# Performance work log

Hardware: AMD Instinct MI355X
Metric: run time of the kernel (lower is better)

Reference implementation:

```python
import jax, jax.numpy as jnp
import numpy as np

EMBED_DIM = 1024
NUM_HEADS = 16
HEAD_DIM = EMBED_DIM // NUM_HEADS
LN_EPS = 1e-5


def setup_inputs() -> dict:
    key = jax.random.key(0)
    ks = jax.random.split(key, 6)
    b, s, d = 2, 2048, EMBED_DIM
    scale = 1.0 / np.sqrt(d)
    x = jax.random.normal(ks[0], (b, s, d), dtype=jnp.float32)
    w_qkv = jax.random.normal(ks[1], (d, 3 * d), dtype=jnp.float32) * scale
    b_qkv = jax.random.normal(ks[2], (3 * d,), dtype=jnp.float32) * 0.02
    w_out = jax.random.normal(ks[3], (d, d), dtype=jnp.float32) * scale
    b_out = jax.random.normal(ks[4], (d,), dtype=jnp.float32) * 0.02
    gamma = jnp.ones((d,), dtype=jnp.float32)
    ln_beta = jnp.zeros((d,), dtype=jnp.float32)
    beta = jax.random.normal(ks[5], (), dtype=jnp.float32) * 0.1
    return {"x": x, "w_qkv": w_qkv, "b_qkv": b_qkv, "w_out": w_out,
            "b_out": b_out, "gamma": gamma, "ln_beta": ln_beta, "beta": beta}


def _layernorm(x, gamma, ln_beta):
    mu = jnp.mean(x, axis=-1, keepdims=True)
    var = jnp.mean(jnp.square(x - mu), axis=-1, keepdims=True)
    return (x - mu) * jax.lax.rsqrt(var + LN_EPS) * gamma + ln_beta


def reference(x, w_qkv, b_qkv, w_out, b_out, gamma, ln_beta, beta):
    b, s, d = x.shape
    h, hd = NUM_HEADS, HEAD_DIM
    residual = x
    xn = _layernorm(x, gamma, ln_beta)
    qkv = xn @ w_qkv + b_qkv                       # [b, s, 3d]
    qkv = qkv.reshape(b, s, 3, h, hd)
    q = jnp.transpose(qkv[:, :, 0], (0, 2, 1, 3))  # [b, h, s, hd]
    k = jnp.transpose(qkv[:, :, 1], (0, 2, 1, 3))
    v = jnp.transpose(qkv[:, :, 2], (0, 2, 1, 3))
    attn = jnp.einsum('bhqd,bhkd->bhqk', q, k) / np.sqrt(hd)
    idx = jnp.arange(s)
    dist = jnp.abs(idx[None, :] - idx[:, None]).astype(attn.dtype)  # [s, s]
    attn = attn + beta * jnp.log1p(dist)[None, None, :, :]
    probs = jax.nn.softmax(attn, axis=-1)
    ctx = jnp.einsum('bhqk,bhkd->bhqd', probs, v)  # [b, h, s, hd]
    ctx = jnp.transpose(ctx, (0, 2, 1, 3)).reshape(b, s, d)
    return residual + ctx @ w_out + b_out
```

## Files before the change

### kernel.cpp

```cpp
#include <hip/hip_runtime.h>

#define SEQ 2048
#define DIM 1024
#define NHEAD 16
#define HDIM 64
#define NTOK 4096
#define N3D 3072

typedef __attribute__((ext_vector_type(8))) short bf16x8;
typedef __attribute__((ext_vector_type(4))) float floatx4;
typedef __attribute__((ext_vector_type(4))) unsigned short ushortx4;

__device__ __forceinline__ unsigned short f2bf(float f) {
    unsigned int u = __builtin_bit_cast(unsigned int, f);
    u += 0x7FFFu + ((u >> 16) & 1u);
    return (unsigned short)(u >> 16);
}

__device__ __forceinline__ void async_copy16(const void* g, const void* l) {
    __builtin_amdgcn_global_load_lds(
        (const __attribute__((address_space(1))) unsigned int*)(unsigned long long)g,
        (__attribute__((address_space(3))) unsigned int*)(unsigned int)(unsigned long long)l,
        16, 0, 0);
}

#define MFMA_BF16(a, b, c) __builtin_amdgcn_mfma_f32_16x16x32_bf16((a), (b), (c), 0, 0, 0)

__global__ __launch_bounds__(256)
void prep_kernel(const float* __restrict__ w_qkv, unsigned short* __restrict__ wqkvT,
                 const float* __restrict__ w_out, unsigned short* __restrict__ woutT,
                 const float* __restrict__ x, const float* __restrict__ gamma,
                 const float* __restrict__ lnb, unsigned short* __restrict__ xn,
                 const float* __restrict__ betap, float* __restrict__ logt_g) {
    const int bid = blockIdx.x;
    const int tid = threadIdx.x;
    if (bid >= 8192) {
        const float betaV = betap[0];
        const float L2E = 1.44269504f;
        int i = (bid - 8192) * 256 + tid;
        logt_g[i] = betaV * log1pf((float)i) * L2E - 20.0f;
        logt_g[i + 1024] = betaV * log1pf((float)(i + 1024)) * L2E - 20.0f;
        return;
    }
    if (bid < 4096) {
        __shared__ float tile[32][33];
        const float* src; unsigned short* dst; int cols, bx, by;
        if (bid < 3072) { src = w_qkv; dst = wqkvT; cols = N3D; bx = bid % 96; by = bid / 96; }
        else { int t = bid - 3072; src = w_out; dst = woutT; cols = DIM; bx = t & 31; by = t >> 5; }
        const int c0 = bx * 32, r0 = by * 32;
        const int tx = tid & 31, ty = tid >> 5;
        for (int i = 0; i < 4; ++i) {
            int r = ty + i * 8;
            tile[r][tx] = src[(size_t)(r0 + r) * cols + c0 + tx];
        }
        __syncthreads();
        for (int i = 0; i < 4; ++i) {
            int rr = ty + i * 8;
            dst[(size_t)(c0 + rr) * DIM + r0 + tx] = f2bf(tile[tx][rr]);
        }
    } else {
        const int row = bid - 4096;
        const float* xr = x + (size_t)row * DIM;
        float4 v = ((const float4*)xr)[tid];
        float s = v.x + v.y + v.z + v.w;
        float s2 = v.x * v.x + v.y * v.y + v.z * v.z + v.w * v.w;
        for (int off = 1; off < 64; off <<= 1) {
            s += __shfl_xor(s, off, 64);
            s2 += __shfl_xor(s2, off, 64);
        }
        __shared__ float red[8];
        const int wave = tid >> 6, lane = tid & 63;
        if (lane == 0) { red[wave] = s; red[4 + wave] = s2; }
        __syncthreads();
        s = red[0] + red[1] + red[2] + red[3];
        s2 = red[4] + red[5] + red[6] + red[7];
        const float mu = s * (1.0f / DIM);
        const float var = s2 * (1.0f / DIM) - mu * mu;
        const float rstd = rsqrtf(var + 1e-5f);
        float4 g = ((const float4*)gamma)[tid];
        float4 bb = ((const float4*)lnb)[tid];
        unsigned short* o = xn + (size_t)row * DIM + tid * 4;
        o[0] = f2bf((v.x - mu) * rstd * g.x + bb.x);
        o[1] = f2bf((v.y - mu) * rstd * g.y + bb.y);
        o[2] = f2bf((v.z - mu) * rstd * g.z + bb.z);
        o[3] = f2bf((v.w - mu) * rstd * g.w + bb.w);
    }
}

__global__ __launch_bounds__(512)
void qkv_gemm(const unsigned short* __restrict__ A, const unsigned short* __restrict__ Bt,
              const float* __restrict__ bias, unsigned short* __restrict__ qo,
              unsigned short* __restrict__ ko, unsigned short* __restrict__ vTo) {
    __shared__ unsigned short Asm[2][256 * 64];
    __shared__ unsigned short Bsm[2][192 * 64];
    const int tid = threadIdx.x;
    const int wave = tid >> 6, lane = tid & 63;
    const int quad = lane >> 4, r16 = lane & 15;
    const int flat = blockIdx.x;
    const int xcd = flat & 7, c = flat >> 3;
    const int mt = (xcd >> 1) * 4 + (c >> 3);
    const int nt = (xcd & 1) * 8 + (c & 7);
    const int m0 = mt * 256, n0 = nt * 192;
    const int wm = (wave & 1) * 128, wn = (wave >> 1) * 48;
    floatx4 acc[8][3] = {};
    for (int p = 0; p < 4; ++p) {
        int s = tid + p * 512;
        async_copy16(A + (size_t)(m0 + (s >> 3)) * DIM + ((s & 7) << 3), &Asm[0][s * 8]);
    }
    for (int p = 0; p < 3; ++p) {
        int s = tid + p * 512;
        async_copy16(Bt + (size_t)(n0 + (s >> 3)) * DIM + ((s & 7) << 3), &Bsm[0][s * 8]);
    }
    __syncthreads();
    for (int it = 0; it < 16; ++it) {
        const int cur = it & 1;
        if (it + 1 < 16) {
            const int k1 = (it + 1) * 64;
            for (int p = 0; p < 4; ++p) {
                int s = tid + p * 512;
                async_copy16(A + (size_t)(m0 + (s >> 3)) * DIM + k1 + ((s & 7) << 3),
                             &Asm[cur ^ 1][s * 8]);
            }
            for (int p = 0; p < 3; ++p) {
                int s = tid + p * 512;
                async_copy16(Bt + (size_t)(n0 + (s >> 3)) * DIM + k1 + ((s & 7) << 3),
                             &Bsm[cur ^ 1][s * 8]);
            }
        }
        for (int h = 0; h < 2; ++h) {
            bf16x8 af[8], bfr[3];
            for (int i = 0; i < 8; ++i)
                af[i] = *(const bf16x8*)(&Asm[cur][(wm + i * 16 + r16) * 64 + h * 32 + quad * 8]);
            for (int j = 0; j < 3; ++j)
                bfr[j] = *(const bf16x8*)(&Bsm[cur][(wn + j * 16 + r16) * 64 + h * 32 + quad * 8]);
            for (int i = 0; i < 8; ++i)
                for (int j = 0; j < 3; ++j)
                    acc[i][j] = MFMA_BF16(af[i], bfr[j], acc[i][j]);
        }
        __syncthreads();
    }
    for (int j = 0; j < 3; ++j) {
        int n = n0 + wn + j * 16 + r16;
        float bn = bias[n];
        int part = n >> 10, nn = n & 1023;
        int head = nn >> 6, hdi = nn & 63;
        for (int i = 0; i < 8; ++i) {
            int mbase = m0 + wm + i * 16 + quad * 4;
            int bIdx = mbase >> 11, sIdx = mbase & 2047;
            if (part == 2) {
                ushortx4 pack;
                for (int e = 0; e < 4; ++e) pack[e] = f2bf(acc[i][j][e] + bn);
                *(ushortx4*)(vTo + ((size_t)(bIdx * NHEAD + head) * HDIM + hdi) * SEQ + sIdx) = pack;
            } else {
                unsigned short* dst = (part == 0) ? qo : ko;
                for (int e = 0; e < 4; ++e)
                    dst[((size_t)(bIdx * NHEAD + head) * SEQ + sIdx + e) * HDIM + hdi] =
                        f2bf(acc[i][j][e] + bn);
            }
        }
    }
}

__global__ __launch_bounds__(512)
void attn_kernel(const unsigned short* __restrict__ qg, const unsigned short* __restrict__ kg,
                 const unsigned short* __restrict__ vTg, const float* __restrict__ logt,
                 unsigned short* __restrict__ ctx) {
    __shared__ unsigned short QP[128][72];
    __shared__ unsigned short Kd[2][64 * 64];
    __shared__ unsigned short Vd[2][64 * 64];

    const int tid = threadIdx.x;
    const int wave = tid >> 6, lane = tid & 63;
    const int quad = lane >> 4, r16 = lane & 15;
    const int flat = blockIdx.y * 16 + blockIdx.x;
    const int swz = (flat & 7) * 64 + (flat >> 3);
    const int bh = swz >> 4, qt = swz & 15;
    const int qBase = qt * 128;
    const float L2E = 1.44269504f;
    const float c1 = 0.125f * L2E;

    const unsigned short* qptr = qg + ((size_t)bh * SEQ + qBase) * HDIM;
    for (int s = tid; s < 1024; s += 512) {
        int r = s >> 3, c8 = (s & 7) << 3;
        *(bf16x8*)(&QP[r][c8]) = *(const bf16x8*)(qptr + r * HDIM + c8);
    }

    const int sr = tid >> 3;
    const int scg = (tid & 7) ^ (sr & 7);
    const unsigned short* kbh = kg + (size_t)bh * SEQ * HDIM;
    const unsigned short* vbh = vTg + (size_t)bh * HDIM * SEQ;
    async_copy16(kbh + (size_t)sr * HDIM + scg * 8, &Kd[0][tid * 8]);
    async_copy16(vbh + (size_t)sr * SEQ + scg * 8, &Vd[0][tid * 8]);
    __syncthreads();

    bf16x8 qf0 = *(const bf16x8*)(&QP[wave * 16 + r16][quad * 8]);
    bf16x8 qf1 = *(const bf16x8*)(&QP[wave * 16 + r16][32 + quad * 8]);

    const bf16x8 onesv = {0x3F80, 0x3F80, 0x3F80, 0x3F80, 0x3F80, 0x3F80, 0x3F80, 0x3F80};

    floatx4 o[5] = {};
    const int qWaveBase = qBase + wave * 16;
    const int qrT = qWaveBase + r16;

    for (int kt0 = 0; kt0 < SEQ; kt0 += 64) {
        const int buf = (kt0 >> 6) & 1;
        if (kt0 + 64 < SEQ) {
            async_copy16(kbh + (size_t)(kt0 + 64 + sr) * HDIM + scg * 8, &Kd[buf ^ 1][tid * 8]);
            async_copy16(vbh + (size_t)sr * SEQ + kt0 + 64 + scg * 8, &Vd[buf ^ 1][tid * 8]);
        }

        floatx4 sc[4];
        __builtin_amdgcn_s_setprio(1);
        for (int ct = 0; ct < 4; ++ct) {
            int rK = ct * 16 + r16;
            const unsigned short* kb = &Kd[buf][rK * 64];
            bf16x8 kf0 = *(const bf16x8*)(kb + ((quad ^ (rK & 7)) << 3));
            bf16x8 kf1 = *(const bf16x8*)(kb + (((quad ^ 4) ^ (rK & 7)) << 3));
            floatx4 z = {0.f, 0.f, 0.f, 0.f};
            z = MFMA_BF16(kf0, qf0, z);
            z = MFMA_BF16(kf1, qf1, z);
            sc[ct] = z;
        }
        __builtin_amdgcn_s_setprio(0);
        for (int ct = 0; ct < 4; ++ct) {
            const int keyTile = kt0 + ct * 16;
            const int kbase = keyTile + quad * 4;
            if (qWaveBase >= keyTile + 16) {
                const float* lp = &logt[qrT - kbase - 3];
                for (int i = 0; i < 4; ++i)
                    sc[ct][i] = __builtin_amdgcn_exp2f(sc[ct][i] * c1 + lp[3 - i]);
            } else if (keyTile >= qWaveBase + 16) {
                const float* lp = &logt[kbase - qrT];
                for (int i = 0; i < 4; ++i)
                    sc[ct][i] = __builtin_amdgcn_exp2f(sc[ct][i] * c1 + lp[i]);
            } else {
                for (int i = 0; i < 4; ++i) {
                    int dist = qrT - (kbase + i);
                    dist = dist < 0 ? -dist : dist;
                    sc[ct][i] = __builtin_amdgcn_exp2f(sc[ct][i] * c1 + logt[dist]);
                }
            }
        }
        {
            unsigned short* prow = &QP[wave * 16 + r16][0];
            for (int ct = 0; ct < 4; ++ct) {
                unsigned int lo, hi;
                asm("v_cvt_pk_bf16_f32 %0, %1, %2" : "=v"(lo) : "v"(sc[ct][0]), "v"(sc[ct][1]));
                asm("v_cvt_pk_bf16_f32 %0, %1, %2" : "=v"(hi) : "v"(sc[ct][2]), "v"(sc[ct][3]));
                uint2 pk; pk.x = lo; pk.y = hi;
                *(uint2*)(prow + ct * 16 + quad * 4) = pk;
            }
        }
        bf16x8 pf0 = *(const bf16x8*)(&QP[wave * 16 + r16][quad * 8]);
        bf16x8 pf1 = *(const bf16x8*)(&QP[wave * 16 + r16][32 + quad * 8]);
        __builtin_amdgcn_s_setprio(1);
        for (int nt = 0; nt < 4; ++nt) {
            int rV = nt * 16 + r16;
            const unsigned short* vb = &Vd[buf][rV * 64];
            bf16x8 vf0 = *(const bf16x8*)(vb + ((quad ^ (rV & 7)) << 3));
            bf16x8 vf1 = *(const bf16x8*)(vb + (((quad ^ 4) ^ (rV & 7)) << 3));
            o[nt] = MFMA_BF16(pf0, vf0, o[nt]);
            o[nt] = MFMA_BF16(pf1, vf1, o[nt]);
        }
        o[4] = MFMA_BF16(pf0, onesv, o[4]);
        o[4] = MFMA_BF16(pf1, onesv, o[4]);
        __builtin_amdgcn_s_setprio(0);

        __syncthreads();
    }

    const int b_ = bh >> 4, h_ = bh & 15;
    for (int i = 0; i < 4; ++i) {
        float inv = 1.0f / o[4][i];
        int qi = qBase + wave * 16 + quad * 4 + i;
        for (int nt = 0; nt < 4; ++nt) {
            int d = nt * 16 + r16;
            ctx[((size_t)(b_ * SEQ + qi)) * DIM + h_ * HDIM + d] = f2bf(o[nt][i] * inv);
        }
    }
}

__global__ __launch_bounds__(256)
void out_gemm(const unsigned short* __restrict__ A, const unsigned short* __restrict__ Bt,
              const float* __restrict__ bias, const float* __restrict__ resid,
              float* __restrict__ out) {
    __shared__ unsigned short Asm[2][128 * 64];
    __shared__ unsigned short Bsm[2][64 * 64];
    const int tid = threadIdx.x;
    const int wave = tid >> 6, lane = tid & 63;
    const int quad = lane >> 4, r16 = lane & 15;
    const int flat = blockIdx.y * 16 + blockIdx.x;
    const int swz = (flat & 7) * 64 + (flat >> 3);
    const int m0 = (swz >> 4) * 128, n0 = (swz & 15) * 64;
    const int wm = (wave & 1) * 64, wn = (wave >> 1) * 32;
    floatx4 acc[4][2] = {};
    for (int p = 0; p < 4; ++p) {
        int s = tid + p * 256;
        async_copy16(A + (size_t)(m0 + (s >> 3)) * DIM + ((s & 7) << 3), &Asm[0][s * 8]);
    }
    for (int p = 0; p < 2; ++p) {
        int s = tid + p * 256;
        async_copy16(Bt + (size_t)(n0 + (s >> 3)) * DIM + ((s & 7) << 3), &Bsm[0][s * 8]);
    }
    __syncthreads();
    for (int it = 0; it < 16; ++it) {
        const int cur = it & 1;
        if (it + 1 < 16) {
            const int k1 = (it + 1) * 64;
            for (int p = 0; p < 4; ++p) {
                int s = tid + p * 256;
                async_copy16(A + (size_t)(m0 + (s >> 3)) * DIM + k1 + ((s & 7) << 3),
                             &Asm[cur ^ 1][s * 8]);
            }
            for (int p = 0; p < 2; ++p) {
                int s = tid + p * 256;
                async_copy16(Bt + (size_t)(n0 + (s >> 3)) * DIM + k1 + ((s & 7) << 3),
                             &Bsm[cur ^ 1][s * 8]);
            }
        }
        for (int h = 0; h < 2; ++h) {
            bf16x8 af[4], bfr[2];
            for (int i = 0; i < 4; ++i)
                af[i] = *(const bf16x8*)(&Asm[cur][(wm + i * 16 + r16) * 64 + h * 32 + quad * 8]);
            for (int j = 0; j < 2; ++j)
                bfr[j] = *(const bf16x8*)(&Bsm[cur][(wn + j * 16 + r16) * 64 + h * 32 + quad * 8]);
            for (int i = 0; i < 4; ++i)
                for (int j = 0; j < 2; ++j)
                    acc[i][j] = MFMA_BF16(af[i], bfr[j], acc[i][j]);
        }
        __syncthreads();
    }
    for (int i = 0; i < 4; ++i)
        for (int j = 0; j < 2; ++j)
            for (int e = 0; e < 4; ++e) {
                int m = m0 + wm + i * 16 + quad * 4 + e;
                int n = n0 + wn + j * 16 + r16;
                out[(size_t)m * DIM + n] = acc[i][j][e] + bias[n] + resid[(size_t)m * DIM + n];
            }
}

extern "C" void kernel_launch(void* const* d_in, const int* in_sizes, int n_in,
                              void* d_out, int out_size, void* d_ws, size_t ws_size,
                              hipStream_t stream) {
    const float* x     = (const float*)d_in[0];
    const float* w_qkv = (const float*)d_in[1];
    const float* b_qkv = (const float*)d_in[2];
    const float* w_out = (const float*)d_in[3];
    const float* b_out = (const float*)d_in[4];
    const float* gamma = (const float*)d_in[5];
    const float* ln_b  = (const float*)d_in[6];
    const float* beta  = (const float*)d_in[7];
    float* out = (float*)d_out;

    char* ws = (char*)d_ws;
    const size_t MB = 1u << 20;
    unsigned short* xn    = (unsigned short*)(ws);
    unsigned short* wqkvT = (unsigned short*)(ws + 8 * MB);
    unsigned short* woutT = (unsigned short*)(ws + 14 * MB);
    unsigned short* qb    = (unsigned short*)(ws + 16 * MB);
    unsigned short* kb    = (unsigned short*)(ws + 24 * MB);
    unsigned short* vTb   = (unsigned short*)(ws + 32 * MB);
    float* logt_g         = (float*)(ws + 40 * MB);
    unsigned short* ctx   = xn;

    prep_kernel<<<8196, 256, 0, stream>>>(w_qkv, wqkvT, w_out, woutT, x, gamma, ln_b, xn,
                                          beta, logt_g);
    qkv_gemm<<<256, 512, 0, stream>>>(xn, wqkvT, b_qkv, qb, kb, vTb);
    attn_kernel<<<dim3(SEQ / 128, 32), 512, 0, stream>>>(qb, kb, vTb, logt_g, ctx);
    out_gemm<<<dim3(16, 32), 256, 0, stream>>>(ctx, woutT, b_out, x, out);
}
```

Measured before the change: 203.0 us.

## Process 32 query rows per wave in attention to reuse K/V fragments

Doubles the query tile per block to 256 rows, so each wave computes two 16-row query groups against the same K/V tiles loaded from LDS. Q fragments are loaded straight from global memory into registers instead of being staged through shared memory. The grid is halved to 256 blocks. The aim is to cut LDS reads and global K/V traffic per unit of work. In exchange, register pressure is higher and there are fewer blocks to hide latency.

```diff
diff --git a/kernel.cpp b/kernel.cpp
--- a/kernel.cpp
+++ b/kernel.cpp
@@ -165,25 +165,26 @@
 void attn_kernel(const unsigned short* __restrict__ qg, const unsigned short* __restrict__ kg,
                  const unsigned short* __restrict__ vTg, const float* __restrict__ logt,
                  unsigned short* __restrict__ ctx) {
-    __shared__ unsigned short QP[128][72];
+    __shared__ unsigned short QP[256][72];
     __shared__ unsigned short Kd[2][64 * 64];
     __shared__ unsigned short Vd[2][64 * 64];
 
     const int tid = threadIdx.x;
     const int wave = tid >> 6, lane = tid & 63;
     const int quad = lane >> 4, r16 = lane & 15;
-    const int flat = blockIdx.y * 16 + blockIdx.x;
-    const int swz = (flat & 7) * 64 + (flat >> 3);
-    const int bh = swz >> 4, qt = swz & 15;
-    const int qBase = qt * 128;
+    const int flat = blockIdx.x;
+    const int swz = (flat & 7) * 32 + (flat >> 3);
+    const int bh = swz >> 3, qt = swz & 7;
+    const int qBase = qt * 256;
     const float L2E = 1.44269504f;
     const float c1 = 0.125f * L2E;
 
     const unsigned short* qptr = qg + ((size_t)bh * SEQ + qBase) * HDIM;
-    for (int s = tid; s < 1024; s += 512) {
-        int r = s >> 3, c8 = (s & 7) << 3;
-        *(bf16x8*)(&QP[r][c8]) = *(const bf16x8*)(qptr + r * HDIM + c8);
-    }
+    const int qr0 = wave * 32 + r16;
+    bf16x8 qf0a = *(const bf16x8*)(qptr + qr0 * HDIM + quad * 8);
+    bf16x8 qf1a = *(const bf16x8*)(qptr + qr0 * HDIM + 32 + quad * 8);
+    bf16x8 qf0b = *(const bf16x8*)(qptr + (qr0 + 16) * HDIM + quad * 8);
+    bf16x8 qf1b = *(const bf16x8*)(qptr + (qr0 + 16) * HDIM + 32 + quad * 8);
 
     const int sr = tid >> 3;
     const int scg = (tid & 7) ^ (sr & 7);
@@ -193,14 +194,15 @@
     async_copy16(vbh + (size_t)sr * SEQ + scg * 8, &Vd[0][tid * 8]);
     __syncthreads();
 
-    bf16x8 qf0 = *(const bf16x8*)(&QP[wave * 16 + r16][quad * 8]);
-    bf16x8 qf1 = *(const bf16x8*)(&QP[wave * 16 + r16][32 + quad * 8]);
-
     const bf16x8 onesv = {0x3F80, 0x3F80, 0x3F80, 0x3F80, 0x3F80, 0x3F80, 0x3F80, 0x3F80};
 
-    floatx4 o[5] = {};
-    const int qWaveBase = qBase + wave * 16;
-    const int qrT = qWaveBase + r16;
+    floatx4 oa[5] = {}, ob[5] = {};
+    const int qWB0 = qBase + wave * 32;
+    const int qWB1 = qWB0 + 16;
+    const int qrTa = qWB0 + r16;
+    const int qrTb = qWB1 + r16;
+    unsigned short* prowA = &QP[wave * 32 + r16][0];
+    unsigned short* prowB = &QP[wave * 32 + 16 + r16][0];
 
     for (int kt0 = 0; kt0 < SEQ; kt0 += 64) {
         const int buf = (kt0 >> 6) & 1;
@@ -209,40 +211,52 @@
             async_copy16(vbh + (size_t)sr * SEQ + kt0 + 64 + scg * 8, &Vd[buf ^ 1][tid * 8]);
         }
 
-        floatx4 sc[4];
-        __builtin_amdgcn_s_setprio(1);
+        bf16x8 kf0[4], kf1[4];
         for (int ct = 0; ct < 4; ++ct) {
             int rK = ct * 16 + r16;
             const unsigned short* kb = &Kd[buf][rK * 64];
-            bf16x8 kf0 = *(const bf16x8*)(kb + ((quad ^ (rK & 7)) << 3));
-            bf16x8 kf1 = *(const bf16x8*)(kb + (((quad ^ 4) ^ (rK & 7)) << 3));
+            kf0[ct] = *(const bf16x8*)(kb + ((quad ^ (rK & 7)) << 3));
+            kf1[ct] = *(const bf16x8*)(kb + (((quad ^ 4) ^ (rK & 7)) << 3));
+        }
+
+        floatx4 sca[4], scb[4];
+        __builtin_amdgcn_s_setprio(1);
+        for (int ct = 0; ct < 4; ++ct) {
             floatx4 z = {0.f, 0.f, 0.f, 0.f};
-            z = MFMA_BF16(kf0, qf0, z);
-            z = MFMA_BF16(kf1, qf1, z);
-            sc[ct] = z;
+            z = MFMA_BF16(kf0[ct], qf0a, z);
+            z = MFMA_BF16(kf1[ct], qf1a, z);
+            sca[ct] = z;
+            floatx4 w = {0.f, 0.f, 0.f, 0.f};
+            w = MFMA_BF16(kf0[ct], qf0b, w);
+            w = MFMA_BF16(kf1[ct], qf1b, w);
+            scb[ct] = w;
         }
         __builtin_amdgcn_s_setprio(0);
-        for (int ct = 0; ct < 4; ++ct) {
-            const int keyTile = kt0 + ct * 16;
-            const int kbase = keyTile + quad * 4;
-            if (qWaveBase >= keyTile + 16) {
-                const float* lp = &logt[qrT - kbase - 3];
-                for (int i = 0; i < 4; ++i)
-                    sc[ct][i] = __builtin_amdgcn_exp2f(sc[ct][i] * c1 + lp[3 - i]);
-            } else if (keyTile >= qWaveBase + 16) {
-                const float* lp = &logt[kbase - qrT];
-                for (int i = 0; i < 4; ++i)
-                    sc[ct][i] = __builtin_amdgcn_exp2f(sc[ct][i] * c1 + lp[i]);
-            } else {
-                for (int i = 0; i < 4; ++i) {
-                    int dist = qrT - (kbase + i);
-                    dist = dist < 0 ? -dist : dist;
-                    sc[ct][i] = __builtin_amdgcn_exp2f(sc[ct][i] * c1 + logt[dist]);
+
+        for (int g = 0; g < 2; ++g) {
+            floatx4* sc = g ? scb : sca;
+            const int qWB = g ? qWB1 : qWB0;
+            const int qrT = g ? qrTb : qrTa;
+            unsigned short* prow = g ? prowB : prowA;
+            for (int ct = 0; ct < 4; ++ct) {
+                const int keyTile = kt0 + ct * 16;
+                const int kbase = keyTile + quad * 4;
+                if (qWB >= keyTile + 16) {
+                    const float* lp = &logt[qrT - kbase - 3];
+                    for (int i = 0; i < 4; ++i)
+                        sc[ct][i] = __builtin_amdgcn_exp2f(sc[ct][i] * c1 + lp[3 - i]);
+                } else if (keyTile >= qWB + 16) {
+                    const float* lp = &logt[kbase - qrT];
+                    for (int i = 0; i < 4; ++i)
+                        sc[ct][i] = __builtin_amdgcn_exp2f(sc[ct][i] * c1 + lp[i]);
+                } else {
+                    for (int i = 0; i < 4; ++i) {
+                        int dist = qrT - (kbase + i);
+                        dist = dist < 0 ? -dist : dist;
+                        sc[ct][i] = __builtin_amdgcn_exp2f(sc[ct][i] * c1 + logt[dist]);
+                    }
                 }
             }
-        }
-        {
-            unsigned short* prow = &QP[wave * 16 + r16][0];
             for (int ct = 0; ct < 4; ++ct) {
                 unsigned int lo, hi;
                 asm("v_cvt_pk_bf16_f32 %0, %1, %2" : "=v"(lo) : "v"(sc[ct][0]), "v"(sc[ct][1]));
@@ -251,19 +265,25 @@
                 *(uint2*)(prow + ct * 16 + quad * 4) = pk;
             }
         }
-        bf16x8 pf0 = *(const bf16x8*)(&QP[wave * 16 + r16][quad * 8]);
-        bf16x8 pf1 = *(const bf16x8*)(&QP[wave * 16 + r16][32 + quad * 8]);
+        bf16x8 pf0a = *(const bf16x8*)(prowA + quad * 8);
+        bf16x8 pf1a = *(const bf16x8*)(prowA + 32 + quad * 8);
+        bf16x8 pf0b = *(const bf16x8*)(prowB + quad * 8);
+        bf16x8 pf1b = *(const bf16x8*)(prowB + 32 + quad * 8);
         __builtin_amdgcn_s_setprio(1);
         for (int nt = 0; nt < 4; ++nt) {
             int rV = nt * 16 + r16;
             const unsigned short* vb = &Vd[buf][rV * 64];
             bf16x8 vf0 = *(const bf16x8*)(vb + ((quad ^ (rV & 7)) << 3));
             bf16x8 vf1 = *(const bf16x8*)(vb + (((quad ^ 4) ^ (rV & 7)) << 3));
-            o[nt] = MFMA_BF16(pf0, vf0, o[nt]);
-            o[nt] = MFMA_BF16(pf1, vf1, o[nt]);
-        }
-        o[4] = MFMA_BF16(pf0, onesv, o[4]);
-        o[4] = MFMA_BF16(pf1, onesv, o[4]);
+            oa[nt] = MFMA_BF16(pf0a, vf0, oa[nt]);
+            oa[nt] = MFMA_BF16(pf1a, vf1, oa[nt]);
+            ob[nt] = MFMA_BF16(pf0b, vf0, ob[nt]);
+            ob[nt] = MFMA_BF16(pf1b, vf1, ob[nt]);
+        }
+        oa[4] = MFMA_BF16(pf0a, onesv, oa[4]);
+        oa[4] = MFMA_BF16(pf1a, onesv, oa[4]);
+        ob[4] = MFMA_BF16(pf0b, onesv, ob[4]);
+        ob[4] = MFMA_BF16(pf1b, onesv, ob[4]);
         __builtin_amdgcn_s_setprio(0);
 
         __syncthreads();
@@ -271,11 +291,14 @@
 
     const int b_ = bh >> 4, h_ = bh & 15;
     for (int i = 0; i < 4; ++i) {
-        float inv = 1.0f / o[4][i];
-        int qi = qBase + wave * 16 + quad * 4 + i;
+        float inva = 1.0f / oa[4][i];
+        float invb = 1.0f / ob[4][i];
+        int qiA = qBase + wave * 32 + quad * 4 + i;
+        int qiB = qiA + 16;
         for (int nt = 0; nt < 4; ++nt) {
             int d = nt * 16 + r16;
-            ctx[((size_t)(b_ * SEQ + qi)) * DIM + h_ * HDIM + d] = f2bf(o[nt][i] * inv);
+            ctx[((size_t)(b_ * SEQ + qiA)) * DIM + h_ * HDIM + d] = f2bf(oa[nt][i] * inva);
+            ctx[((size_t)(b_ * SEQ + qiB)) * DIM + h_ * HDIM + d] = f2bf(ob[nt][i] * invb);
         }
     }
 }
@@ -366,6 +389,6 @@
     prep_kernel<<<8196, 256, 0, stream>>>(w_qkv, wqkvT, w_out, woutT, x, gamma, ln_b, xn,
                                           beta, logt_g);
     qkv_gemm<<<256, 512, 0, stream>>>(xn, wqkvT, b_qkv, qb, kb, vTb);
-    attn_kernel<<<dim3(SEQ / 128, 32), 512, 0, stream>>>(qb, kb, vTb, logt_g, ctx);
+    attn_kernel<<<256, 512, 0, stream>>>(qb, kb, vTb, logt_g, ctx);
     out_gemm<<<dim3(16, 32), 256, 0, stream>>>(ctx, woutT, b_out, x, out);
 }
```

New measurement: 219.3 us. +8.0%, slower.
